# Kernel optimization log

Measured on AMD Instinct MI355X. Metric: run time of the kernel, lower is better.

## Reference

```python
import jax, jax.numpy as jnp
import numpy as np

B, S, D, H = 2, 2048, 1024, 16
DK = D // H  # 64, even -> RoPE valid


def _rotate_half(x):
    # torch: stack((-x[...,1::2], x[...,::2]), -1).flatten(-2) -> interleaved
    x1 = x[..., 0::2]
    x2 = x[..., 1::2]
    return jnp.stack((-x2, x1), axis=-1).reshape(x.shape)


def _build_rope(seq_len, d_k, dtype=jnp.float32):
    inv_freq = 1.0 / (10000.0 ** (jnp.arange(0, d_k, 2, dtype=dtype) / d_k))
    pos = jnp.arange(seq_len, dtype=dtype)
    angles = pos[:, None] * inv_freq[None, :]  # [S, d_k/2]
    sin = jnp.repeat(jnp.sin(angles), 2, axis=-1)  # [S, d_k]
    cos = jnp.repeat(jnp.cos(angles), 2, axis=-1)
    return cos, sin


def _apply_rope(x, cos, sin):
    # x: [B, H, S, d_k]; cos/sin: [S, d_k]
    return x * cos[None, None] + _rotate_half(x) * sin[None, None]


def setup_inputs():
    key = jax.random.key(0)
    ks = jax.random.split(key, 11)
    s = 0.02
    inp = {
        'Q': jax.random.normal(ks[0], (B, S, D), jnp.float32),
        'K': jax.random.normal(ks[1], (B, S, D), jnp.float32),
        'V': jax.random.normal(ks[2], (B, S, D), jnp.float32),
        'Wq': jax.random.normal(ks[3], (D, D), jnp.float32) * s,
        'bq': jnp.zeros((D,), jnp.float32),
        'Wk': jax.random.normal(ks[4], (D, D), jnp.float32) * s,
        'bk': jnp.zeros((D,), jnp.float32),
        'Wv': jax.random.normal(ks[5], (D, D), jnp.float32) * s,
        'bv': jnp.zeros((D,), jnp.float32),
        'Wo': jax.random.normal(ks[6], (D, D), jnp.float32) * s,
        'bo': jnp.zeros((D,), jnp.float32),
        # causal mask, broadcast over batch
        'mask': jnp.broadcast_to(jnp.tril(jnp.ones((S, S), jnp.int32))[None, None], (B, 1, S, S)),
    }
    return inp


def reference(Q, K, V, Wq, bq, Wk, bk, Wv, bv, Wo, bo, mask):
    # projections (torch Linear: x @ W.T + b), split heads -> [B, H, S, d_k]
    def proj(x, W, b):
        return (x @ W.T + b).reshape(B, -1, H, DK).transpose(0, 2, 1, 3)

    q = proj(Q, Wq, bq)
    k = proj(K, Wk, bk)
    v = proj(V, Wv, bv)

    cos, sin = _build_rope(S, DK)
    q = _apply_rope(q, cos, sin)
    k = _apply_rope(k, cos, sin)

    scores = jnp.einsum('bhqd,bhkd->bhqk', q, k) / jnp.sqrt(jnp.float32(DK))
    scores = jnp.where(mask == 0, -jnp.inf, scores)
    attn = jax.nn.softmax(scores, axis=-1)  # dropout is identity in eval / p=0
    out = jnp.einsum('bhqk,bhkd->bhqd', attn, v)  # [B, H, S, d_k]
    out = out.transpose(0, 2, 1, 3).reshape(B, -1, D)
    out = out @ Wo.T + bo
    return out, attn
```

## Files before the change

### kernel.cpp

```cpp
#include <hip/hip_runtime.h>
#include <math.h>

namespace {
constexpr int Bn  = 2;
constexpr int Sn  = 2048;
constexpr int Dn  = 1024;
constexpr int Hn  = 16;
constexpr int DKn = 64;
constexpr int Mn  = Bn * Sn;
}

typedef __attribute__((ext_vector_type(8))) short short8;
typedef __attribute__((ext_vector_type(4))) float f32x4;
typedef __attribute__((ext_vector_type(8))) unsigned short ushort8v;

__device__ __forceinline__ unsigned short f2bf(float x) {
  union { float f; unsigned u; } un; un.f = x;
  unsigned r = un.u + 0x7fffu + ((un.u >> 16) & 1u);
  return (unsigned short)(r >> 16);
}

__device__ __forceinline__ void async_copy16(const void* g, void* l) {
  __builtin_amdgcn_global_load_lds(
      (const __attribute__((address_space(1))) unsigned int*)g,
      (__attribute__((address_space(3))) unsigned int*)l, 16, 0, 0);
}

__device__ __forceinline__ int swz(int row, int ch) {
  return row * 64 + (((ch) ^ (row & 7)) << 3);
}

__global__ __launch_bounds__(256)
void cvt_bf16_kernel(const float* s0, const float* s1, const float* s2,
                     const float* s3, const float* s4, const float* s5,
                     const float* s6,
                     unsigned short* d0, unsigned short* d1, unsigned short* d2,
                     unsigned short* d3, unsigned short* d4, unsigned short* d5,
                     unsigned short* d6) {
  const int which = blockIdx.y;
  const float* s;
  unsigned short* d;
  int n;
  switch (which) {
    case 0: s = s0; d = d0; n = Mn * Dn; break;
    case 1: s = s1; d = d1; n = Mn * Dn; break;
    case 2: s = s2; d = d2; n = Mn * Dn; break;
    case 3: s = s3; d = d3; n = Dn * Dn; break;
    case 4: s = s4; d = d4; n = Dn * Dn; break;
    case 5: s = s5; d = d5; n = Dn * Dn; break;
    default: s = s6; d = d6; n = Dn * Dn; break;
  }
  int idx = (blockIdx.x * 256 + threadIdx.x) * 4;
  if (idx >= n) return;
  float4 v = *(const float4*)(s + idx);
  ushort4 o;
  o.x = f2bf(v.x); o.y = f2bf(v.y); o.z = f2bf(v.z); o.w = f2bf(v.w);
  *(ushort4*)(d + idx) = o;
}

__global__ void rope_table_kernel(float* __restrict__ cost, float* __restrict__ sint) {
  int s = blockIdx.x;
  int i = threadIdx.x;
  double inv_freq = pow(10000.0, -(double)(2 * i) / 64.0);
  double ang = (double)s * inv_freq;
  cost[s * 32 + i] = (float)cos(ang);
  sint[s * 32 + i] = (float)sin(ang);
}

__device__ __forceinline__ void gemm_bf16_core(const unsigned short* __restrict__ A,
                                               const unsigned short* __restrict__ B,
                                               int m0, int n0, int K, int tid,
                                               f32x4 (&acc)[4][4]) {
  __shared__ unsigned short As[128 * 32];
  __shared__ unsigned short Bs[128 * 32];
  const int lane = tid & 63, wave = tid >> 6;
  const int wrow = (wave >> 1) * 64, wcol = (wave & 1) * 64;
  const int lx = lane & 15, quad = lane >> 4;

  for (int k0 = 0; k0 < K; k0 += 32) {
    __syncthreads();
#pragma unroll
    for (int c = 0; c < 2; ++c) {
      int slot = wave * 128 + c * 64 + lane;
      int row = slot >> 2, ch = slot & 3;
      async_copy16(A + (size_t)(m0 + row) * K + k0 + ch * 8,
                   &As[(size_t)(wave * 128 + c * 64) * 8]);
      async_copy16(B + (size_t)(n0 + row) * K + k0 + ch * 8,
                   &Bs[(size_t)(wave * 128 + c * 64) * 8]);
    }
    __syncthreads();
    short8 af[4], bf[4];
#pragma unroll
    for (int i = 0; i < 4; ++i)
      af[i] = *(const short8*)&As[(wrow + i * 16 + lx) * 32 + quad * 8];
#pragma unroll
    for (int j = 0; j < 4; ++j)
      bf[j] = *(const short8*)&Bs[(wcol + j * 16 + lx) * 32 + quad * 8];
#pragma unroll
    for (int i = 0; i < 4; ++i)
#pragma unroll
      for (int j = 0; j < 4; ++j)
        acc[i][j] = __builtin_amdgcn_mfma_f32_16x16x32_bf16(af[i], bf[j], acc[i][j], 0, 0, 0);
  }
}

__global__ __launch_bounds__(256)
void qkv_mfma_kernel(const unsigned short* __restrict__ Xq,
                     const unsigned short* __restrict__ Xk,
                     const unsigned short* __restrict__ Xv,
                     const unsigned short* __restrict__ Wqb,
                     const unsigned short* __restrict__ Wkb,
                     const unsigned short* __restrict__ Wvb,
                     const float* __restrict__ bq, const float* __restrict__ bk,
                     const float* __restrict__ bv,
                     const float* __restrict__ cost, const float* __restrict__ sint,
                     unsigned short* __restrict__ qb, unsigned short* __restrict__ kb,
                     unsigned short* __restrict__ vtb) {
  const int which = blockIdx.z;
  const unsigned short* A  = which == 0 ? Xq  : which == 1 ? Xk  : Xv;
  const unsigned short* Bw = which == 0 ? Wqb : which == 1 ? Wkb : Wvb;
  const float* bias        = which == 0 ? bq  : which == 1 ? bk  : bv;
  unsigned short* outp     = which == 0 ? qb  : which == 1 ? kb  : vtb;
  const int m0 = blockIdx.x * 128, n0 = blockIdx.y * 128;
  const int tid = threadIdx.x, lane = tid & 63, wave = tid >> 6;
  const int wrow = (wave >> 1) * 64, wcol = (wave & 1) * 64;
  const int lx = lane & 15, quad = lane >> 4;

  __shared__ unsigned short tb[32][136];

  f32x4 acc[4][4];
#pragma unroll
  for (int i = 0; i < 4; ++i)
#pragma unroll
    for (int j = 0; j < 4; ++j) acc[i][j] = (f32x4){0.f, 0.f, 0.f, 0.f};

  gemm_bf16_core(A, Bw, m0, n0, 1024, tid, acc);

  if (which < 2) {
#pragma unroll
    for (int ni = 0; ni < 4; ++ni) {
      const int gn = n0 + wcol + ni * 16 + lx;
      const int h = gn >> 6, dk = gn & 63;
      const float bb = bias[gn];
      const int pi = dk >> 1;
      const float sgn = (dk & 1) ? 1.f : -1.f;
#pragma unroll
      for (int mi = 0; mi < 4; ++mi) {
#pragma unroll
        for (int r = 0; r < 4; ++r) {
          const int gm = m0 + wrow + mi * 16 + quad * 4 + r;
          const int b = gm >> 11, spos = gm & 2047;
          float v = acc[mi][ni][r] + bb;
          float partner = __shfl_xor(v, 1, 64);
          float c = cost[spos * 32 + pi], s = sint[spos * 32 + pi];
          v = v * c + sgn * partner * s;
          outp[((size_t)(b * Hn + h) * Sn + spos) * DKn + dk] = f2bf(v);
        }
      }
    }
  } else {
    const int bb_ = m0 >> 11;
    const int sp0 = m0 & 2047;
#pragma unroll
    for (int s = 0; s < 4; ++s) {
      __syncthreads();
      const bool mine = (wcol == 0) ? (s < 2) : (s >= 2);
      if (mine) {
        const int nia = (s & 1) * 2;
#pragma unroll
        for (int np = 0; np < 2; ++np) {
          const int ni = nia + np;
          const int fl = np * 16 + lx;
          const float bbv = bias[n0 + s * 32 + fl];
#pragma unroll
          for (int mi = 0; mi < 4; ++mi)
#pragma unroll
            for (int r = 0; r < 4; ++r) {
              const int tok = wrow + mi * 16 + quad * 4 + r;
              tb[fl][tok] = f2bf(acc[mi][ni][r] + bbv);
            }
        }
      }
      __syncthreads();
#pragma unroll
      for (int it = 0; it < 2; ++it) {
        const int e = it * 256 + tid;
        const int f = e >> 4, ch = e & 15;
        const int gn = n0 + s * 32 + f;
        const int hh = gn >> 6, dk = gn & 63;
        ushort8v val = *(const ushort8v*)&tb[f][ch * 8];
        *(ushort8v*)(outp + ((size_t)(bb_ * Hn + hh) * DKn + dk) * Sn + sp0 + ch * 8) = val;
      }
    }
  }
}

__global__ __launch_bounds__(256)
void attn_mfma_kernel(const unsigned short* __restrict__ qb,
                      const unsigned short* __restrict__ kb,
                      const unsigned short* __restrict__ vtb,
                      float* __restrict__ attn_out, unsigned short* __restrict__ ob) {
  const int wg = blockIdx.x;
  const int xcd = wg & 7, j = wg >> 3;
  const int bh = xcd * 4 + (j >> 5);
  const int qt = 31 - (j & 31);
  const int b = bh >> 4, h = bh & 15;
  const size_t hoff = (size_t)bh * (Sn * DKn);
  const unsigned short* Qh  = qb  + hoff + (size_t)qt * 64 * DKn;
  const unsigned short* Kh  = kb  + hoff;
  const unsigned short* VTh = vtb + hoff;
  float* attn = attn_out + (size_t)bh * Sn * Sn;

  __shared__ unsigned short ps[64 * 64];

  const int tid = threadIdx.x, lane = tid & 63, wave = tid >> 6;
  const int quad = lane >> 4, lx = lane & 15;
  const int r0 = qt * 64;
  const float scale = 0.125f;
  const int qrow = wave * 16 + lx;

  short8 aq[2];
#pragma unroll
  for (int ksc = 0; ksc < 2; ++ksc)
    aq[ksc] = *(const short8*)(Qh + (size_t)qrow * DKn + (ksc * 4 + quad) * 8);

  float lsum[4] = {0.f, 0.f, 0.f, 0.f};
  for (int kt = 0; kt <= qt; ++kt) {
#pragma unroll
    for (int c = 0; c < 4; ++c) {
      if (kt == qt && c > wave) continue;
      f32x4 s4 = (f32x4){0.f, 0.f, 0.f, 0.f};
      const int krow = kt * 64 + c * 16 + lx;
#pragma unroll
      for (int ksc = 0; ksc < 2; ++ksc) {
        short8 bk8 = *(const short8*)(Kh + (size_t)krow * DKn + (ksc * 4 + quad) * 8);
        s4 = __builtin_amdgcn_mfma_f32_16x16x32_bf16(aq[ksc], bk8, s4, 0, 0, 0);
      }
      const int ct = c * 16 + lx;
#pragma unroll
      for (int r = 0; r < 4; ++r) {
        const int rt = wave * 16 + quad * 4 + r;
        float p = (kt == qt && ct > rt) ? 0.f : __expf(s4[r] * scale);
        lsum[r] += p;
      }
    }
  }
#pragma unroll
  for (int off = 1; off < 16; off <<= 1)
#pragma unroll
    for (int r = 0; r < 4; ++r) lsum[r] += __shfl_xor(lsum[r], off, 64);
  float inv_l[4];
#pragma unroll
  for (int r = 0; r < 4; ++r) inv_l[r] = 1.f / lsum[r];

  f32x4 oacc[4];
#pragma unroll
  for (int c = 0; c < 4; ++c) oacc[c] = (f32x4){0.f, 0.f, 0.f, 0.f};

  for (int kt = 0; kt <= qt; ++kt) {
#pragma unroll
    for (int c = 0; c < 4; ++c) {
      f32x4 s4 = (f32x4){0.f, 0.f, 0.f, 0.f};
      const int krow = kt * 64 + c * 16 + lx;
#pragma unroll
      for (int ksc = 0; ksc < 2; ++ksc) {
        short8 bk8 = *(const short8*)(Kh + (size_t)krow * DKn + (ksc * 4 + quad) * 8);
        s4 = __builtin_amdgcn_mfma_f32_16x16x32_bf16(aq[ksc], bk8, s4, 0, 0, 0);
      }
      const int ct = c * 16 + lx;
      const int pch = (ct >> 3);
#pragma unroll
      for (int r = 0; r < 4; ++r) {
        const int rt = wave * 16 + quad * 4 + r;
        float p = (kt == qt && ct > rt) ? 0.f : __expf(s4[r] * scale) * inv_l[r];
        __builtin_nontemporal_store(p, &attn[(size_t)(r0 + rt) * Sn + kt * 64 + ct]);
        ps[rt * 64 + ((pch ^ (rt & 7)) << 3) + (ct & 7)] = f2bf(p);
      }
    }
    asm volatile("s_waitcnt lgkmcnt(0)" ::: "memory");
    __builtin_amdgcn_sched_barrier(0);

    short8 ap[2];
#pragma unroll
    for (int ksc = 0; ksc < 2; ++ksc)
      ap[ksc] = *(const short8*)&ps[swz(qrow, quad + ksc * 4)];
#pragma unroll
    for (int c2 = 0; c2 < 4; ++c2) {
      const int vrow = c2 * 16 + lx;
#pragma unroll
      for (int ksc = 0; ksc < 2; ++ksc) {
        short8 bv8 = *(const short8*)(VTh + (size_t)vrow * Sn + kt * 64 + ksc * 32 + quad * 8);
        oacc[c2] = __builtin_amdgcn_mfma_f32_16x16x32_bf16(ap[ksc], bv8, oacc[c2], 0, 0, 0);
      }
    }
  }

#pragma unroll
  for (int c2 = 0; c2 < 4; ++c2) {
#pragma unroll
    for (int r = 0; r < 4; ++r) {
      const int grow = r0 + wave * 16 + quad * 4 + r;
      const int dk = c2 * 16 + lx;
      ob[((size_t)(b * Sn) + grow) * Dn + h * 64 + dk] = f2bf(oacc[c2][r]);
    }
  }

  const f32x4 z = (f32x4){0.f, 0.f, 0.f, 0.f};
  for (int kt = qt + 1; kt < 32; ++kt) {
#pragma unroll
    for (int it = 0; it < 4; ++it) {
      int e = it * 256 + tid;
      int row = e >> 4, c4 = e & 15;
      __builtin_nontemporal_store(
          z, (f32x4*)(attn + (size_t)(r0 + row) * Sn + kt * 64 + c4 * 4));
    }
  }
}

__global__ __launch_bounds__(256)
void outproj_mfma_kernel(const unsigned short* __restrict__ Ob,
                         const unsigned short* __restrict__ Wob,
                         const float* __restrict__ bo, float* __restrict__ out) {
  const int m0 = blockIdx.x * 128, n0 = blockIdx.y * 128;
  const int tid = threadIdx.x, lane = tid & 63, wave = tid >> 6;
  const int wrow = (wave >> 1) * 64, wcol = (wave & 1) * 64;
  const int lx = lane & 15, quad = lane >> 4;

  f32x4 acc[4][4];
#pragma unroll
  for (int i = 0; i < 4; ++i)
#pragma unroll
    for (int j = 0; j < 4; ++j) acc[i][j] = (f32x4){0.f, 0.f, 0.f, 0.f};

  gemm_bf16_core(Ob, Wob, m0, n0, 1024, tid, acc);

#pragma unroll
  for (int ni = 0; ni < 4; ++ni) {
    const int gn = n0 + wcol + ni * 16 + lx;
    const float bb = bo[gn];
#pragma unroll
    for (int mi = 0; mi < 4; ++mi) {
#pragma unroll
      for (int r = 0; r < 4; ++r) {
        const int gm = m0 + wrow + mi * 16 + quad * 4 + r;
        out[(size_t)gm * Dn + gn] = acc[mi][ni][r] + bb;
      }
    }
  }
}

extern "C" void kernel_launch(void* const* d_in, const int* in_sizes, int n_in,
                              void* d_out, int out_size, void* d_ws, size_t ws_size,
                              hipStream_t stream) {
  (void)in_sizes; (void)n_in; (void)out_size; (void)ws_size;
  const float* Q  = (const float*)d_in[0];
  const float* K  = (const float*)d_in[1];
  const float* V  = (const float*)d_in[2];
  const float* Wq = (const float*)d_in[3];
  const float* bq = (const float*)d_in[4];
  const float* Wk = (const float*)d_in[5];
  const float* bk = (const float*)d_in[6];
  const float* Wv = (const float*)d_in[7];
  const float* bv = (const float*)d_in[8];
  const float* Wo = (const float*)d_in[9];
  const float* bo = (const float*)d_in[10];

  float* out  = (float*)d_out;
  float* attn = out + (size_t)Mn * Dn;

  unsigned short* w = (unsigned short*)d_ws;
  unsigned short* Xqb = w;
  unsigned short* Xkb = Xqb + (size_t)Mn * Dn;
  unsigned short* Xvb = Xkb + (size_t)Mn * Dn;
  unsigned short* Wqb = Xvb + (size_t)Mn * Dn;
  unsigned short* Wkb = Wqb + (size_t)Dn * Dn;
  unsigned short* Wvb = Wkb + (size_t)Dn * Dn;
  unsigned short* Wob = Wvb + (size_t)Dn * Dn;
  unsigned short* qb  = Wob + (size_t)Dn * Dn;
  unsigned short* kb  = qb + (size_t)Mn * Dn;
  unsigned short* vtb = kb + (size_t)Mn * Dn;
  unsigned short* ob  = vtb + (size_t)Mn * Dn;
  float* cost = (float*)(ob + (size_t)Mn * Dn);
  float* sint = cost + (size_t)Sn * 32;

  cvt_bf16_kernel<<<dim3(4096, 7), dim3(256), 0, stream>>>(
      Q, K, V, Wq, Wk, Wv, Wo, Xqb, Xkb, Xvb, Wqb, Wkb, Wvb, Wob);
  rope_table_kernel<<<dim3(Sn), dim3(32), 0, stream>>>(cost, sint);
  qkv_mfma_kernel<<<dim3(32, 8, 3), dim3(256), 0, stream>>>(
      Xqb, Xkb, Xvb, Wqb, Wkb, Wvb, bq, bk, bv, cost, sint, qb, kb, vtb);
  attn_mfma_kernel<<<dim3(1024), dim3(256), 0, stream>>>(qb, kb, vtb, attn, ob);
  outproj_mfma_kernel<<<dim3(32, 8), dim3(256), 0, stream>>>(ob, Wob, bo, out);
}
```

Before: 888.0 us.

## Stage K and V tiles through LDS with async copies in attention kernel

The attention kernel now loads each 64x64 K tile (and the V^T tile in the second pass) into swizzled shared memory with async global-to-LDS copies, and all four waves read from there instead of each wave fetching K/V directly from global memory. This is meant to cut redundant global/L2 traffic and give the MFMA operand reads the swizzled LDS pattern. The launch grid also changes from a 1D XCD-aware mapping to a plain 3D (qtile, head, batch) grid, which drops the explicit L2 locality grouping per XCD. The change adds two barriers per key tile and does no double buffering, so load latency is exposed.

```diff
diff --git a/kernel.cpp b/kernel.cpp
--- a/kernel.cpp
+++ b/kernel.cpp
@@ -200,17 +200,16 @@
                       const unsigned short* __restrict__ kb,
                       const unsigned short* __restrict__ vtb,
                       float* __restrict__ attn_out, unsigned short* __restrict__ ob) {
-  const int wg = blockIdx.x;
-  const int xcd = wg & 7, j = wg >> 3;
-  const int bh = xcd * 4 + (j >> 5);
-  const int qt = 31 - (j & 31);
-  const int b = bh >> 4, h = bh & 15;
-  const size_t hoff = (size_t)bh * (Sn * DKn);
+  const int qt = 31 - blockIdx.x;
+  const int h = blockIdx.y, b = blockIdx.z;
+  const size_t hoff = (size_t)(b * Hn + h) * Sn * DKn;
   const unsigned short* Qh  = qb  + hoff + (size_t)qt * 64 * DKn;
   const unsigned short* Kh  = kb  + hoff;
   const unsigned short* VTh = vtb + hoff;
-  float* attn = attn_out + (size_t)bh * Sn * Sn;
-
+  float* attn = attn_out + (size_t)(b * Hn + h) * Sn * Sn;
+
+  __shared__ unsigned short ks[64 * 64];
+  __shared__ unsigned short vs[64 * 64];
   __shared__ unsigned short ps[64 * 64];
 
   const int tid = threadIdx.x, lane = tid & 63, wave = tid >> 6;
@@ -219,6 +218,9 @@
   const float scale = 0.125f;
   const int qrow = wave * 16 + lx;
 
+  const int srow = (tid & 255) >> 3;
+  const int sch  = tid & 7;
+
   short8 aq[2];
 #pragma unroll
   for (int ksc = 0; ksc < 2; ++ksc)
@@ -226,14 +228,22 @@
 
   float lsum[4] = {0.f, 0.f, 0.f, 0.f};
   for (int kt = 0; kt <= qt; ++kt) {
+    __syncthreads();
+#pragma unroll
+    for (int it = 0; it < 2; ++it) {
+      const int row = it * 32 + srow;
+      async_copy16(Kh + (size_t)(kt * 64 + row) * 64 + ((sch ^ (row & 7)) << 3),
+                   &ks[(it * 256 + (tid & ~63)) * 8]);
+    }
+    __syncthreads();
 #pragma unroll
     for (int c = 0; c < 4; ++c) {
       if (kt == qt && c > wave) continue;
       f32x4 s4 = (f32x4){0.f, 0.f, 0.f, 0.f};
-      const int krow = kt * 64 + c * 16 + lx;
+      const int krow = c * 16 + lx;
 #pragma unroll
       for (int ksc = 0; ksc < 2; ++ksc) {
-        short8 bk8 = *(const short8*)(Kh + (size_t)krow * DKn + (ksc * 4 + quad) * 8);
+        short8 bk8 = *(const short8*)&ks[swz(krow, ksc * 4 + quad)];
         s4 = __builtin_amdgcn_mfma_f32_16x16x32_bf16(aq[ksc], bk8, s4, 0, 0, 0);
       }
       const int ct = c * 16 + lx;
@@ -258,13 +268,24 @@
   for (int c = 0; c < 4; ++c) oacc[c] = (f32x4){0.f, 0.f, 0.f, 0.f};
 
   for (int kt = 0; kt <= qt; ++kt) {
+    __syncthreads();
+#pragma unroll
+    for (int it = 0; it < 2; ++it) {
+      const int row = it * 32 + srow;
+      async_copy16(Kh + (size_t)(kt * 64 + row) * 64 + ((sch ^ (row & 7)) << 3),
+                   &ks[(it * 256 + (tid & ~63)) * 8]);
+      async_copy16(VTh + (size_t)row * Sn + kt * 64 + ((sch ^ (row & 7)) << 3),
+                   &vs[(it * 256 + (tid & ~63)) * 8]);
+    }
+    __syncthreads();
+
 #pragma unroll
     for (int c = 0; c < 4; ++c) {
       f32x4 s4 = (f32x4){0.f, 0.f, 0.f, 0.f};
-      const int krow = kt * 64 + c * 16 + lx;
+      const int krow = c * 16 + lx;
 #pragma unroll
       for (int ksc = 0; ksc < 2; ++ksc) {
-        short8 bk8 = *(const short8*)(Kh + (size_t)krow * DKn + (ksc * 4 + quad) * 8);
+        short8 bk8 = *(const short8*)&ks[swz(krow, ksc * 4 + quad)];
         s4 = __builtin_amdgcn_mfma_f32_16x16x32_bf16(aq[ksc], bk8, s4, 0, 0, 0);
       }
       const int ct = c * 16 + lx;
@@ -283,13 +304,13 @@
     short8 ap[2];
 #pragma unroll
     for (int ksc = 0; ksc < 2; ++ksc)
-      ap[ksc] = *(const short8*)&ps[swz(qrow, quad + ksc * 4)];
+      ap[ksc] = *(const short8*)&ps[swz(qrow, ksc * 4 + quad)];
 #pragma unroll
     for (int c2 = 0; c2 < 4; ++c2) {
       const int vrow = c2 * 16 + lx;
 #pragma unroll
       for (int ksc = 0; ksc < 2; ++ksc) {
-        short8 bv8 = *(const short8*)(VTh + (size_t)vrow * Sn + kt * 64 + ksc * 32 + quad * 8);
+        short8 bv8 = *(const short8*)&vs[swz(vrow, ksc * 4 + quad)];
         oacc[c2] = __builtin_amdgcn_mfma_f32_16x16x32_bf16(ap[ksc], bv8, oacc[c2], 0, 0, 0);
       }
     }
@@ -388,6 +409,6 @@
   rope_table_kernel<<<dim3(Sn), dim3(32), 0, stream>>>(cost, sint);
   qkv_mfma_kernel<<<dim3(32, 8, 3), dim3(256), 0, stream>>>(
       Xqb, Xkb, Xvb, Wqb, Wkb, Wvb, bq, bk, bv, cost, sint, qb, kb, vtb);
-  attn_mfma_kernel<<<dim3(1024), dim3(256), 0, stream>>>(qb, kb, vtb, attn, ob);
+  attn_mfma_kernel<<<dim3(32, Hn, Bn), dim3(256), 0, stream>>>(qb, kb, vtb, attn, ob);
   outproj_mfma_kernel<<<dim3(32, 8), dim3(256), 0, stream>>>(ob, Wob, bo, out);
 }
```

Measured after the change: 794.8 us. 1.12x faster.
